# Kernel optimization log

Measured on AMD Instinct MI355X. Metric: run time of the kernel, lower is better.

## Reference

```python
import jax, jax.numpy as jnp
import numpy as np
import math

B, S, D, H = 2, 2048, 1024, 16
HD = D // H  # head_dims = 64


def setup_inputs() -> dict:
    key = jax.random.key(0)
    ks = jax.random.split(key, 8)
    sc = 1.0 / math.sqrt(D)
    return {
        "queries": jax.random.normal(ks[0], (B, S, D), jnp.float32),
        "keys":    jax.random.normal(ks[1], (B, S, D), jnp.float32),
        "values":  jax.random.normal(ks[2], (B, S, D), jnp.float32),
        # causal mask: 1 where attending allowed, 0 where blocked (masked_fill on ==0)
        "mask": jnp.tril(jnp.ones((S, S), jnp.int32)),
        "Wq": jax.random.normal(ks[3], (D, D), jnp.float32) * sc,
        "bq": jnp.zeros((D,), jnp.float32),
        "Wk": jax.random.normal(ks[4], (D, D), jnp.float32) * sc,
        "bk": jnp.zeros((D,), jnp.float32),
        "Wv": jax.random.normal(ks[5], (D, D), jnp.float32) * sc,
        "bv": jnp.zeros((D,), jnp.float32),
        "Wo": jax.random.normal(ks[6], (D, D), jnp.float32) * sc,
        "bo": jnp.zeros((D,), jnp.float32),
    }


def _split_heads(x):
    # (B, S, D) -> (B, H, S, HD)
    return x.reshape(B, S, H, HD).transpose(0, 2, 1, 3)


def reference(queries, keys, values, mask, Wq, bq, Wk, bk, Wv, bv, Wo, bo):
    q = queries @ Wq + bq
    k = keys @ Wk + bk
    # NOTE: faithful to source quirk — V is projected from the ALREADY-PROJECTED keys
    # (original: keys = self.W_keys(keys); values = self.W_values(keys))
    v = k @ Wv + bv
    q, k, v = _split_heads(q), _split_heads(k), _split_heads(v)
    # naive full NxN attention, as in the source
    scores = jnp.einsum("bhqd,bhkd->bhqk", q, k) / math.sqrt(HD)
    scores = jnp.where(mask == 0, jnp.float32(-1e9), scores)
    probs = jax.nn.softmax(scores, axis=-1)
    attn = jnp.einsum("bhqk,bhkd->bhqd", probs, v)
    attn = attn.transpose(0, 2, 1, 3).reshape(B, S, D)
    return attn @ Wo + bo
```

## Files before the change

### kernel.cpp

```cpp
#include <hip/hip_runtime.h>

typedef unsigned short u16;
typedef unsigned int u32;
typedef __bf16 bf16x8 __attribute__((ext_vector_type(8)));
typedef float f32x4 __attribute__((ext_vector_type(4)));

#define MFMA16(a, b, c) __builtin_amdgcn_mfma_f32_16x16x32_bf16(a, b, c, 0, 0, 0)

__device__ __forceinline__ void gload16(const void* g, void* l) {
  __builtin_amdgcn_global_load_lds((const __attribute__((address_space(1))) void*)g,
                                   (__attribute__((address_space(3))) void*)l, 16, 0, 0);
}

__device__ __forceinline__ u16 f2bf(float f) {
  u32 u = __builtin_bit_cast(u32, f);
  u += 0x7fffu + ((u >> 16) & 1u);
  return (u16)(u >> 16);
}
__device__ __forceinline__ u32 pack2(float a, float b) {
  return (u32)f2bf(a) | ((u32)f2bf(b) << 16);
}

__global__ __launch_bounds__(256) void cvt_kernel(const float* __restrict__ q,
                                                  const float* __restrict__ k,
                                                  u16* __restrict__ qb,
                                                  u16* __restrict__ kb) {
  const float* src = blockIdx.y ? k : q;
  u16* dst = blockIdx.y ? kb : qb;
  size_t i = (size_t)blockIdx.x * 256 + threadIdx.x;
  float4 v = ((const float4*)src)[i];
  ushort4 o;
  o.x = f2bf(v.x); o.y = f2bf(v.y); o.z = f2bf(v.z); o.w = f2bf(v.w);
  ((ushort4*)dst)[i] = o;
}

__global__ __launch_bounds__(256) void wtrans_kernel(const float* W0, const float* W1,
                                                     const float* W2, const float* W3,
                                                     u16* T0, u16* T1, u16* T2, u16* T3) {
  int z = blockIdx.z;
  const float* W = z == 0 ? W0 : z == 1 ? W1 : z == 2 ? W2 : W3;
  u16* T = z == 0 ? T0 : z == 1 ? T1 : z == 2 ? T2 : T3;
  __shared__ float tile[64][65];
  int tr = blockIdx.y * 64, tc = blockIdx.x * 64;
  int tid = threadIdx.x;
  int c4 = (tid & 15) * 4, r0 = tid >> 4;
#pragma unroll
  for (int i = 0; i < 4; i++) {
    int r = r0 + i * 16;
    float4 v = *(const float4*)(W + (size_t)(tr + r) * 1024 + tc + c4);
    tile[r][c4 + 0] = v.x; tile[r][c4 + 1] = v.y;
    tile[r][c4 + 2] = v.z; tile[r][c4 + 3] = v.w;
  }
  __syncthreads();
#pragma unroll
  for (int i = 0; i < 2; i++) {
    int c = tid + i * 256;
    int n = c >> 3, kg = c & 7;
    uint4 o;
    o.x = pack2(tile[kg * 8 + 0][n], tile[kg * 8 + 1][n]);
    o.y = pack2(tile[kg * 8 + 2][n], tile[kg * 8 + 3][n]);
    o.z = pack2(tile[kg * 8 + 4][n], tile[kg * 8 + 5][n]);
    o.w = pack2(tile[kg * 8 + 6][n], tile[kg * 8 + 7][n]);
    *(uint4*)(T + (size_t)(tc + n) * 1024 + tr + kg * 8) = o;
  }
}

template <int MODE>
__global__ __launch_bounds__(256) void gemm_kernel(
    const u16* A0, const u16* B0, const float* bias0, void* C0, float scale0,
    const u16* A1, const u16* B1, const float* bias1, void* C1, float scale1,
    int M, int N, int K) {
  const u16* A = A0; const u16* Bt = B0; const float* bias = bias0; void* Cout = C0;
  float scale = scale0;
  if (blockIdx.z) { A = A1; Bt = B1; bias = bias1; Cout = C1; scale = scale1; }

  __shared__ __attribute__((aligned(16))) char sAB[24576];
  char* sA = sAB;
  char* sB = sAB + 16384;
  const int tid = threadIdx.x, lane = tid & 63, w = tid >> 6;
  const int l15 = lane & 15, quad = lane >> 4;
  const int wm = (w >> 1) * 64, wn = (w & 1) * 32;
  const int m0 = blockIdx.y * 128, n0 = blockIdx.x * 64;

  const int lrow = lane >> 3, lcg = (lane & 7) ^ lrow;
  const u16* aP[4]; const u16* bP[2];
  char *lA[4], *lB[2];
#pragma unroll
  for (int i = 0; i < 4; i++) {
    int r = w * 32 + i * 8 + lrow;
    aP[i] = A + (size_t)(m0 + r) * K + lcg * 8;
    lA[i] = sA + w * 4096 + i * 1024;
  }
#pragma unroll
  for (int i = 0; i < 2; i++) {
    int r = w * 16 + i * 8 + lrow;
    bP[i] = Bt + (size_t)(n0 + r) * K + lcg * 8;
    lB[i] = sB + w * 2048 + i * 1024;
  }

  int aoff[4], boff[2];
#pragma unroll
  for (int t = 0; t < 4; t++) {
    int ra = wm + t * 16 + l15;
    aoff[t] = ra * 128 + ((quad ^ (ra & 7)) * 16);
  }
#pragma unroll
  for (int t = 0; t < 2; t++) {
    int rb = wn + t * 16 + l15;
    boff[t] = rb * 128 + ((quad ^ (rb & 7)) * 16);
  }

  f32x4 acc[4][2] = {};
  for (int k = 0; k < K; k += 64) {
    __syncthreads();
#pragma unroll
    for (int i = 0; i < 4; i++) { gload16(aP[i], lA[i]); aP[i] += 64; }
#pragma unroll
    for (int i = 0; i < 2; i++) { gload16(bP[i], lB[i]); bP[i] += 64; }
    __syncthreads();
#pragma unroll
    for (int kt = 0; kt < 2; kt++) {
      bf16x8 af[4], bfr[2];
#pragma unroll
      for (int t = 0; t < 4; t++) af[t] = *(const bf16x8*)(sA + (aoff[t] ^ (kt * 64)));
#pragma unroll
      for (int t = 0; t < 2; t++) bfr[t] = *(const bf16x8*)(sB + (boff[t] ^ (kt * 64)));
#pragma unroll
      for (int mt = 0; mt < 4; mt++)
#pragma unroll
        for (int nt = 0; nt < 2; nt++)
          acc[mt][nt] = MFMA16(af[mt], bfr[nt], acc[mt][nt]);
    }
  }

#pragma unroll
  for (int nt = 0; nt < 2; nt++) {
    int col = n0 + wn + nt * 16 + l15;
    float bv = bias[col];
#pragma unroll
    for (int mt = 0; mt < 4; mt++) {
      int row = m0 + wm + mt * 16 + quad * 4;
      if (MODE == 0) {
        u16* C = (u16*)Cout;
#pragma unroll
        for (int r = 0; r < 4; r++)
          C[(size_t)(row + r) * N + col] = f2bf((acc[mt][nt][r] + bv) * scale);
      } else if (MODE == 1) {
        u16* C = (u16*)Cout;
        int hh = col >> 6, hd = col & 63;
        int bb = row >> 11, s = row & 2047;
        ushort4 o;
        o.x = f2bf((acc[mt][nt][0] + bv) * scale);
        o.y = f2bf((acc[mt][nt][1] + bv) * scale);
        o.z = f2bf((acc[mt][nt][2] + bv) * scale);
        o.w = f2bf((acc[mt][nt][3] + bv) * scale);
        *(ushort4*)(C + ((size_t)((bb * 16 + hh) * 64 + hd) * 2048 + s)) = o;
      } else {
        float* C = (float*)Cout;
#pragma unroll
        for (int r = 0; r < 4; r++)
          C[(size_t)(row + r) * N + col] = (acc[mt][nt][r] + bv) * scale;
      }
    }
  }
}

__global__ __launch_bounds__(256) void attn_kernel(const u16* __restrict__ qw,
                                                   const u16* __restrict__ kw,
                                                   const u16* __restrict__ vw,
                                                   u16* __restrict__ aout) {
  __shared__ __attribute__((aligned(16))) char sQ[8192];
  __shared__ __attribute__((aligned(16))) char sKV[2][16384];
  __shared__ __attribute__((aligned(16))) char sP[8192];
  const int bh = blockIdx.x, p = blockIdx.y;
  const int b = bh >> 4, h = bh & 15;
  const int tid = threadIdx.x, lane = tid & 63, w = tid >> 6;
  const int l15 = lane & 15, quad = lane >> 4;
  const int lrow = lane >> 3, lcg = (lane & 7) ^ lrow;
  const u16* kb0 = kw + (size_t)(b * 2048) * 1024 + h * 64;
  const u16* vb0 = vw + (size_t)bh * 64 * 2048;

  for (int phase = 0; phase < 2; ++phase) {
    const int t = phase ? (31 - p) : p;
    __syncthreads();
    {
      const u16* qbase = qw + (size_t)(b * 2048 + t * 64) * 1024 + h * 64;
#pragma unroll
      for (int i = 0; i < 2; i++) {
        int r = w * 16 + i * 8 + lrow;
        gload16(qbase + (size_t)r * 1024 + lcg * 8, sQ + w * 2048 + i * 1024);
        gload16(kb0 + (size_t)r * 1024 + lcg * 8, sKV[0] + w * 2048 + i * 1024);
        gload16(vb0 + (size_t)r * 2048 + lcg * 8, sKV[0] + 8192 + w * 2048 + i * 1024);
      }
    }

    float lsum = 0.f;
    f32x4 o[4] = {};
    for (int j = 0; j <= t; ++j) {
      __syncthreads();
      const char* sK = sKV[j & 1];
      const char* sV = sK + 8192;

      f32x4 st[4] = {};
#pragma unroll
      for (int kt = 0; kt < 2; ++kt) {
        bf16x8 kf[4], qf;
        {
          int row = w * 16 + l15;
          qf = *(const bf16x8*)(sQ + row * 128 + (((kt * 4 + quad) ^ (row & 7)) * 16));
        }
#pragma unroll
        for (int mt = 0; mt < 4; mt++) {
          int row = mt * 16 + l15;
          kf[mt] = *(const bf16x8*)(sK + row * 128 + (((kt * 4 + quad) ^ (row & 7)) * 16));
        }
#pragma unroll
        for (int mt = 0; mt < 4; mt++) st[mt] = MFMA16(kf[mt], qf, st[mt]);
      }

      const bool dmask = (j == t);
      const int qcol = w * 16 + l15;
      float e[4][4];
#pragma unroll
      for (int mt = 0; mt < 4; mt++)
#pragma unroll
        for (int r = 0; r < 4; r++) {
          float ev = __builtin_amdgcn_exp2f(st[mt][r]);
          if (dmask && (mt * 16 + quad * 4 + r > qcol)) ev = 0.f;
          e[mt][r] = ev;
          lsum += ev;
        }

      {
        int qrow = l15;
#pragma unroll
        for (int mt = 0; mt < 4; mt++) {
          u32 lo = pack2(e[mt][0], e[mt][1]);
          u32 hi = pack2(e[mt][2], e[mt][3]);
          int cgp = (2 * mt + (quad >> 1)) ^ (qrow & 7);
          *(uint2*)(sP + w * 2048 + qrow * 128 + cgp * 16 + (quad & 1) * 8) =
              make_uint2(lo, hi);
        }
      }
      __syncthreads();

      if (j < t) {
        char* dstb = sKV[(j + 1) & 1];
#pragma unroll
        for (int i = 0; i < 2; i++) {
          int r = w * 16 + i * 8 + lrow;
          gload16(kb0 + (size_t)((j + 1) * 64 + r) * 1024 + lcg * 8,
                  dstb + w * 2048 + i * 1024);
          gload16(vb0 + (size_t)r * 2048 + (j + 1) * 64 + lcg * 8,
                  dstb + 8192 + w * 2048 + i * 1024);
        }
      }

#pragma unroll
      for (int kt = 0; kt < 2; ++kt) {
        bf16x8 vf[4], pf;
        {
          int qrow = l15;
          pf = *(const bf16x8*)(sP + w * 2048 + qrow * 128 +
                                (((kt * 4 + quad) ^ (qrow & 7)) * 16));
        }
#pragma unroll
        for (int mt = 0; mt < 4; mt++) {
          int row = mt * 16 + l15;
          vf[mt] = *(const bf16x8*)(sV + row * 128 + (((kt * 4 + quad) ^ (row & 7)) * 16));
        }
#pragma unroll
        for (int mt = 0; mt < 4; mt++) o[mt] = MFMA16(vf[mt], pf, o[mt]);
      }
    }

    lsum += __shfl_xor(lsum, 16, 64);
    lsum += __shfl_xor(lsum, 32, 64);
    float inv = 1.0f / lsum;
    int token = b * 2048 + t * 64 + w * 16 + l15;
#pragma unroll
    for (int mt = 0; mt < 4; mt++) {
      int d0 = h * 64 + mt * 16 + quad * 4;
      ushort4 ov;
      ov.x = f2bf(o[mt][0] * inv);
      ov.y = f2bf(o[mt][1] * inv);
      ov.z = f2bf(o[mt][2] * inv);
      ov.w = f2bf(o[mt][3] * inv);
      *(ushort4*)(aout + (size_t)token * 1024 + d0) = ov;
    }
  }
}

extern "C" void kernel_launch(void* const* d_in, const int* in_sizes, int n_in,
                              void* d_out, int out_size, void* d_ws, size_t ws_size,
                              hipStream_t stream) {
  const float* queries = (const float*)d_in[0];
  const float* keys    = (const float*)d_in[1];
  const float* Wq = (const float*)d_in[4];
  const float* bq = (const float*)d_in[5];
  const float* Wk = (const float*)d_in[6];
  const float* bk = (const float*)d_in[7];
  const float* Wv = (const float*)d_in[8];
  const float* bv = (const float*)d_in[9];
  const float* Wo = (const float*)d_in[10];
  const float* bo = (const float*)d_in[11];

  char* ws = (char*)d_ws;
  u16* qb  = (u16*)(ws);
  u16* kb  = (u16*)(ws + (8u << 20));
  u16* qP  = (u16*)(ws + (16u << 20));
  u16* kP  = (u16*)(ws);
  u16* vP  = (u16*)(ws + (8u << 20));
  u16* WqT = (u16*)(ws + (24u << 20));
  u16* WkT = (u16*)(ws + (26u << 20));
  u16* WvT = (u16*)(ws + (28u << 20));
  u16* WoT = (u16*)(ws + (30u << 20));

  const float kscale = 1.4426950408889634f / 8.0f;

  cvt_kernel<<<dim3(4096, 2), 256, 0, stream>>>(queries, keys, qb, kb);
  wtrans_kernel<<<dim3(16, 16, 4), 256, 0, stream>>>(Wq, Wk, Wv, Wo, WqT, WkT, WvT, WoT);
  gemm_kernel<0><<<dim3(16, 32, 2), 256, 0, stream>>>(
      qb, WqT, bq, qP, kscale, kb, WkT, bk, kP, 1.0f, 4096, 1024, 1024);
  gemm_kernel<1><<<dim3(16, 32, 1), 256, 0, stream>>>(
      kP, WvT, bv, vP, 1.0f, kP, WvT, bv, vP, 1.0f, 4096, 1024, 1024);
  attn_kernel<<<dim3(32, 16), 256, 0, stream>>>(qP, kP, vP, qP);
  gemm_kernel<2><<<dim3(16, 32, 1), 256, 0, stream>>>(
      qP, WoT, bo, d_out, 1.0f, qP, WoT, bo, d_out, 1.0f, 4096, 1024, 1024);
}
```

Measured before the change: 233.7 us.

## Double-buffer GEMM LDS tiles and streamline attention inner loop

The GEMM kernel gets a double-buffered LDS (48KB), so the next K-tile's global-to-LDS load is issued before computing on the current one, and one barrier per iteration is dropped. The attention kernel precomputes swizzled LDS offsets and peels the diagonal (masked) tile out of the main loop. It also removes the per-iteration barrier between writing P and reading it, relying on each wave reading only its own P region. Risks are the higher LDS use lowering GEMM occupancy, and a race if the next-tile prefetch can overwrite a buffer still being read.

```diff
diff --git a/kernel.cpp b/kernel.cpp
--- a/kernel.cpp
+++ b/kernel.cpp
@@ -74,9 +74,7 @@
   float scale = scale0;
   if (blockIdx.z) { A = A1; Bt = B1; bias = bias1; Cout = C1; scale = scale1; }
 
-  __shared__ __attribute__((aligned(16))) char sAB[24576];
-  char* sA = sAB;
-  char* sB = sAB + 16384;
+  __shared__ __attribute__((aligned(16))) char sAB[49152];
   const int tid = threadIdx.x, lane = tid & 63, w = tid >> 6;
   const int l15 = lane & 15, quad = lane >> 4;
   const int wm = (w >> 1) * 64, wn = (w & 1) * 32;
@@ -84,19 +82,12 @@
 
   const int lrow = lane >> 3, lcg = (lane & 7) ^ lrow;
   const u16* aP[4]; const u16* bP[2];
-  char *lA[4], *lB[2];
-#pragma unroll
-  for (int i = 0; i < 4; i++) {
-    int r = w * 32 + i * 8 + lrow;
-    aP[i] = A + (size_t)(m0 + r) * K + lcg * 8;
-    lA[i] = sA + w * 4096 + i * 1024;
-  }
-#pragma unroll
-  for (int i = 0; i < 2; i++) {
-    int r = w * 16 + i * 8 + lrow;
-    bP[i] = Bt + (size_t)(n0 + r) * K + lcg * 8;
-    lB[i] = sB + w * 2048 + i * 1024;
-  }
+#pragma unroll
+  for (int i = 0; i < 4; i++)
+    aP[i] = A + (size_t)(m0 + w * 32 + i * 8 + lrow) * K + lcg * 8;
+#pragma unroll
+  for (int i = 0; i < 2; i++)
+    bP[i] = Bt + (size_t)(n0 + w * 16 + i * 8 + lrow) * K + lcg * 8;
 
   int aoff[4], boff[2];
 #pragma unroll
@@ -107,30 +98,40 @@
 #pragma unroll
   for (int t = 0; t < 2; t++) {
     int rb = wn + t * 16 + l15;
-    boff[t] = rb * 128 + ((quad ^ (rb & 7)) * 16);
-  }
+    boff[t] = 16384 + rb * 128 + ((quad ^ (rb & 7)) * 16);
+  }
+
+#pragma unroll
+  for (int i = 0; i < 4; i++) { gload16(aP[i], sAB + w * 4096 + i * 1024); aP[i] += 64; }
+#pragma unroll
+  for (int i = 0; i < 2; i++) { gload16(bP[i], sAB + 16384 + w * 2048 + i * 1024); bP[i] += 64; }
 
   f32x4 acc[4][2] = {};
+  int cur = 0;
   for (int k = 0; k < K; k += 64) {
     __syncthreads();
-#pragma unroll
-    for (int i = 0; i < 4; i++) { gload16(aP[i], lA[i]); aP[i] += 64; }
-#pragma unroll
-    for (int i = 0; i < 2; i++) { gload16(bP[i], lB[i]); bP[i] += 64; }
-    __syncthreads();
+    if (k + 64 < K) {
+      char* dst = sAB + (cur ^ 1) * 24576;
+#pragma unroll
+      for (int i = 0; i < 4; i++) { gload16(aP[i], dst + w * 4096 + i * 1024); aP[i] += 64; }
+#pragma unroll
+      for (int i = 0; i < 2; i++) { gload16(bP[i], dst + 16384 + w * 2048 + i * 1024); bP[i] += 64; }
+    }
+    const char* buf = sAB + cur * 24576;
 #pragma unroll
     for (int kt = 0; kt < 2; kt++) {
       bf16x8 af[4], bfr[2];
 #pragma unroll
-      for (int t = 0; t < 4; t++) af[t] = *(const bf16x8*)(sA + (aoff[t] ^ (kt * 64)));
-#pragma unroll
-      for (int t = 0; t < 2; t++) bfr[t] = *(const bf16x8*)(sB + (boff[t] ^ (kt * 64)));
+      for (int t = 0; t < 4; t++) af[t] = *(const bf16x8*)(buf + (aoff[t] ^ (kt * 64)));
+#pragma unroll
+      for (int t = 0; t < 2; t++) bfr[t] = *(const bf16x8*)(buf + (boff[t] ^ (kt * 64)));
 #pragma unroll
       for (int mt = 0; mt < 4; mt++)
 #pragma unroll
         for (int nt = 0; nt < 2; nt++)
           acc[mt][nt] = MFMA16(af[mt], bfr[nt], acc[mt][nt]);
     }
+    cur ^= 1;
   }
 
 #pragma unroll
@@ -180,6 +181,24 @@
   const u16* kb0 = kw + (size_t)(b * 2048) * 1024 + h * 64;
   const u16* vb0 = vw + (size_t)bh * 64 * 2048;
 
+  int qoff[2], poff[2], koff[2][4], voff[2][4], wroff[4];
+#pragma unroll
+  for (int kt = 0; kt < 2; kt++) {
+    int qrow = w * 16 + l15;
+    qoff[kt] = qrow * 128 + (((kt * 4 + quad) ^ (qrow & 7)) * 16);
+    poff[kt] = w * 2048 + l15 * 128 + (((kt * 4 + quad) ^ (l15 & 7)) * 16);
+#pragma unroll
+    for (int mt = 0; mt < 4; mt++) {
+      int r2 = mt * 16 + l15;
+      koff[kt][mt] = r2 * 128 + (((kt * 4 + quad) ^ (r2 & 7)) * 16);
+      voff[kt][mt] = 8192 + koff[kt][mt];
+    }
+  }
+#pragma unroll
+  for (int mt = 0; mt < 4; mt++)
+    wroff[mt] = w * 2048 + l15 * 128 + (((2 * mt + (quad >> 1)) ^ (l15 & 7)) * 16) +
+                (quad & 1) * 8;
+
   for (int phase = 0; phase < 2; ++phase) {
     const int t = phase ? (31 - p) : p;
     __syncthreads();
@@ -194,57 +213,11 @@
       }
     }
 
-    float lsum = 0.f;
+    float ls[4] = {0.f, 0.f, 0.f, 0.f};
     f32x4 o[4] = {};
-    for (int j = 0; j <= t; ++j) {
+    for (int j = 0; j < t; ++j) {
       __syncthreads();
-      const char* sK = sKV[j & 1];
-      const char* sV = sK + 8192;
-
-      f32x4 st[4] = {};
-#pragma unroll
-      for (int kt = 0; kt < 2; ++kt) {
-        bf16x8 kf[4], qf;
-        {
-          int row = w * 16 + l15;
-          qf = *(const bf16x8*)(sQ + row * 128 + (((kt * 4 + quad) ^ (row & 7)) * 16));
-        }
-#pragma unroll
-        for (int mt = 0; mt < 4; mt++) {
-          int row = mt * 16 + l15;
-          kf[mt] = *(const bf16x8*)(sK + row * 128 + (((kt * 4 + quad) ^ (row & 7)) * 16));
-        }
-#pragma unroll
-        for (int mt = 0; mt < 4; mt++) st[mt] = MFMA16(kf[mt], qf, st[mt]);
-      }
-
-      const bool dmask = (j == t);
-      const int qcol = w * 16 + l15;
-      float e[4][4];
-#pragma unroll
-      for (int mt = 0; mt < 4; mt++)
-#pragma unroll
-        for (int r = 0; r < 4; r++) {
-          float ev = __builtin_amdgcn_exp2f(st[mt][r]);
-          if (dmask && (mt * 16 + quad * 4 + r > qcol)) ev = 0.f;
-          e[mt][r] = ev;
-          lsum += ev;
-        }
-
       {
-        int qrow = l15;
-#pragma unroll
-        for (int mt = 0; mt < 4; mt++) {
-          u32 lo = pack2(e[mt][0], e[mt][1]);
-          u32 hi = pack2(e[mt][2], e[mt][3]);
-          int cgp = (2 * mt + (quad >> 1)) ^ (qrow & 7);
-          *(uint2*)(sP + w * 2048 + qrow * 128 + cgp * 16 + (quad & 1) * 8) =
-              make_uint2(lo, hi);
-        }
-      }
-      __syncthreads();
-
-      if (j < t) {
         char* dstb = sKV[(j + 1) & 1];
 #pragma unroll
         for (int i = 0; i < 2; i++) {
@@ -255,25 +228,78 @@
                   dstb + 8192 + w * 2048 + i * 1024);
         }
       }
-
+      const char* bufb = sKV[j & 1];
+
+      f32x4 st[4] = {};
 #pragma unroll
       for (int kt = 0; kt < 2; ++kt) {
-        bf16x8 vf[4], pf;
-        {
-          int qrow = l15;
-          pf = *(const bf16x8*)(sP + w * 2048 + qrow * 128 +
-                                (((kt * 4 + quad) ^ (qrow & 7)) * 16));
+        bf16x8 qf = *(const bf16x8*)(sQ + qoff[kt]);
+        bf16x8 kf[4];
+#pragma unroll
+        for (int mt = 0; mt < 4; mt++) kf[mt] = *(const bf16x8*)(bufb + koff[kt][mt]);
+#pragma unroll
+        for (int mt = 0; mt < 4; mt++) st[mt] = MFMA16(kf[mt], qf, st[mt]);
+      }
+#pragma unroll
+      for (int mt = 0; mt < 4; mt++) {
+        float e0 = __builtin_amdgcn_exp2f(st[mt][0]);
+        float e1 = __builtin_amdgcn_exp2f(st[mt][1]);
+        float e2 = __builtin_amdgcn_exp2f(st[mt][2]);
+        float e3 = __builtin_amdgcn_exp2f(st[mt][3]);
+        ls[mt] += (e0 + e1) + (e2 + e3);
+        *(uint2*)(sP + wroff[mt]) = make_uint2(pack2(e0, e1), pack2(e2, e3));
+      }
+      __asm__ volatile("" ::: "memory");
+#pragma unroll
+      for (int kt = 0; kt < 2; ++kt) {
+        bf16x8 pf = *(const bf16x8*)(sP + poff[kt]);
+        bf16x8 vf[4];
+#pragma unroll
+        for (int mt = 0; mt < 4; mt++) vf[mt] = *(const bf16x8*)(bufb + voff[kt][mt]);
+#pragma unroll
+        for (int mt = 0; mt < 4; mt++) o[mt] = MFMA16(vf[mt], pf, o[mt]);
+      }
+    }
+
+    {
+      __syncthreads();
+      const char* bufb = sKV[t & 1];
+      f32x4 st[4] = {};
+#pragma unroll
+      for (int kt = 0; kt < 2; ++kt) {
+        bf16x8 qf = *(const bf16x8*)(sQ + qoff[kt]);
+        bf16x8 kf[4];
+#pragma unroll
+        for (int mt = 0; mt < 4; mt++) kf[mt] = *(const bf16x8*)(bufb + koff[kt][mt]);
+#pragma unroll
+        for (int mt = 0; mt < 4; mt++) st[mt] = MFMA16(kf[mt], qf, st[mt]);
+      }
+      const int qcol = w * 16 + l15;
+#pragma unroll
+      for (int mt = 0; mt < 4; mt++) {
+        float e[4];
+#pragma unroll
+        for (int r = 0; r < 4; r++) {
+          float ev = __builtin_amdgcn_exp2f(st[mt][r]);
+          if (mt * 16 + quad * 4 + r > qcol) ev = 0.f;
+          e[r] = ev;
         }
-#pragma unroll
-        for (int mt = 0; mt < 4; mt++) {
-          int row = mt * 16 + l15;
-          vf[mt] = *(const bf16x8*)(sV + row * 128 + (((kt * 4 + quad) ^ (row & 7)) * 16));
-        }
+        ls[mt] += (e[0] + e[1]) + (e[2] + e[3]);
+        *(uint2*)(sP + wroff[mt]) = make_uint2(pack2(e[0], e[1]), pack2(e[2], e[3]));
+      }
+      __asm__ volatile("" ::: "memory");
+#pragma unroll
+      for (int kt = 0; kt < 2; ++kt) {
+        bf16x8 pf = *(const bf16x8*)(sP + poff[kt]);
+        bf16x8 vf[4];
+#pragma unroll
+        for (int mt = 0; mt < 4; mt++) vf[mt] = *(const bf16x8*)(bufb + voff[kt][mt]);
 #pragma unroll
         for (int mt = 0; mt < 4; mt++) o[mt] = MFMA16(vf[mt], pf, o[mt]);
       }
     }
 
+    float lsum = (ls[0] + ls[1]) + (ls[2] + ls[3]);
     lsum += __shfl_xor(lsum, 16, 64);
     lsum += __shfl_xor(lsum, 32, 64);
     float inv = 1.0f / lsum;
```

Measured after the change: 221.6 us. -5.2%, faster.
